# Optimization experiments

Hardware: AMD Instinct MI355X
Metric: run time of the kernel (lower is better)

Reference implementation:

```python
import jax, jax.numpy as jnp
from jax import lax
import numpy as np

EPS = 1e-8

def squash(x, axis=-1):
    sq = jnp.sum(x * x, axis=axis, keepdims=True)
    return sq / (1.0 + sq) * x / (jnp.sqrt(sq) + EPS)

def conv1d(x, w, b):
    # x: [B, Cin, L], w: [Cout, Cin, K]
    y = lax.conv_general_dilated(x, w, (1,), 'VALID',
                                 dimension_numbers=('NCH', 'OIH', 'NCH'))
    return y + b[None, :, None]

def setup_inputs() -> dict:
    key = jax.random.key(0)
    ks = jax.random.split(key, 6)
    B = 4096
    x = jax.random.normal(ks[0], (B, 50, 128), dtype=jnp.float32)
    conv1_w = jax.random.normal(ks[1], (50, 128, 9), dtype=jnp.float32) * (1.0 / np.sqrt(128 * 9))
    conv1_b = jnp.zeros((50,), dtype=jnp.float32)
    pconv_w = jax.random.normal(ks[2], (64, 42, 3), dtype=jnp.float32) * (1.0 / np.sqrt(42 * 3))
    pconv_b = jnp.zeros((64,), dtype=jnp.float32)
    W = 0.01 * jax.random.normal(ks[3], (5, 384, 16, 8), dtype=jnp.float32)
    return {"x": x, "conv1_w": conv1_w, "conv1_b": conv1_b,
            "pconv_w": pconv_w, "pconv_b": pconv_b, "W": W}

def reference(x, conv1_w, conv1_b, pconv_w, pconv_b, W):
    B = x.shape[0]
    NUM_ROUTING = 3
    # conv + relu: [B,50,128] -> [B,128,50] -> conv -> [B,50,42] -> permute -> [B,42,50]
    h = conv1d(jnp.transpose(x, (0, 2, 1)), conv1_w, conv1_b)
    h = jnp.transpose(jax.nn.relu(h), (0, 2, 1))  # [B,42,50]
    # primary caps: conv1d -> [B,64,48] -> reshape [B,384,8] -> squash
    p = conv1d(h, pconv_w, pconv_b)
    u = squash(p.reshape(B, -1, 8), axis=-1)  # [B,384,8]
    # u_hat[b,o,c,d] = W[o,c,d,i] * u[b,c,i]
    u_hat = jnp.einsum('ocdi,bci->bocd', W, u)  # [B,5,384,16]
    tu = lax.stop_gradient(u_hat)
    b = jnp.zeros((B, 5, 384, 1), dtype=u_hat.dtype)
    for _ in range(NUM_ROUTING - 1):
        c = jax.nn.softmax(b, axis=1)            # [B,5,384,1]
        s = jnp.sum(c * tu, axis=2)              # [B,5,16]
        v = squash(s)                            # [B,5,16]
        uv = jnp.einsum('bocd,bod->boc', tu, v)[..., None]
        b = b + uv
    c = jax.nn.softmax(b, axis=1)
    s = jnp.sum(c * u_hat, axis=2)
    v = squash(s)  # [B,5,16]
    return v
```

## Files before the change

### kernel.cpp

```cpp
#include <hip/hip_runtime.h>
#include <hip/hip_bf16.h>

typedef unsigned short ushort_t;
typedef _Float16 h2 __attribute__((ext_vector_type(2)));
typedef _Float16 half4_t __attribute__((ext_vector_type(4)));
typedef _Float16 half8_t __attribute__((ext_vector_type(8)));
typedef float f32x4 __attribute__((ext_vector_type(4)));
#define EPSQ 1e-8f

__device__ __forceinline__ float fdot2f(h2 a, h2 b, float c) {
#if __has_builtin(__builtin_amdgcn_fdot2)
  return __builtin_amdgcn_fdot2(a, b, c, false);
#else
  return fmaf((float)a.x, (float)b.x, fmaf((float)a.y, (float)b.y, c));
#endif
}
__device__ __forceinline__ h2 bc_h2(unsigned int v) { return __builtin_bit_cast(h2, v); }
__device__ __forceinline__ unsigned int bc_u32(h2 v) { return __builtin_bit_cast(unsigned int, v); }
__device__ __forceinline__ ushort_t bc_u16(_Float16 v) { return __builtin_bit_cast(ushort_t, v); }


__global__ __launch_bounds__(256) void k0_prep(
    const float* __restrict__ w1, const float* __restrict__ pw,
    const float* __restrict__ Wf,
    _Float16* __restrict__ wc16, _Float16* __restrict__ pwB16,
    _Float16* __restrict__ Whs)
{
  int i = blockIdx.x * 256 + threadIdx.x;
  if (i < 73728) {
    int c  = i / 8192;
    int r  = i % 8192;
    int co = r >> 7;
    int k  = r & 127;
    wc16[i] = (co < 50) ? (_Float16)w1[co*1152 + k*9 + c] : (_Float16)0.f;
  }
  if (i < 10240) {
    int co2 = i / 160, kk = i % 160;
    int k = kk / 48, ci = kk % 48;
    float v = (k < 3 && ci < 42) ? pw[co2*126 + ci*3 + k] : 0.f;
    pwB16[i] = (_Float16)v;
  }
  {
    int i8 = i & 7;
    int r  = i >> 3;
    int d  = r & 15;
    int rc = r >> 4;
    int c  = rc % 384;
    int o  = rc / 384;
    Whs[(((o*16 + d)*384) + c)*8 + i8] = (_Float16)Wf[i];
  }
}

__global__ __launch_bounds__(256) void k12_mfma(
    const float* __restrict__ x, const float* __restrict__ b1,
    const float* __restrict__ b2, const _Float16* __restrict__ wc16,
    const _Float16* __restrict__ pwB16, ushort_t* __restrict__ u16)
{
  __shared__ float smem[19728];
  _Float16* xh   = (_Float16*)smem;
  _Float16* hr16 = (_Float16*)smem;
  _Float16* pB   = (_Float16*)smem + 8736;
  float*    pbuf = smem + 9744;

  const int tid   = threadIdx.x;
  const int w     = tid >> 6;
  const int lane  = tid & 63;
  const int lc    = lane & 15;
  const int qd    = lane >> 4;
  const int gbase = blockIdx.x * 3;

  for (int j = tid; j < 4800; j += 256) {
    int g = j / 1600, r = j - g*1600;
    int p = r >> 5, q = r & 31;
    int bb = gbase + g; if (bb > 4095) bb = 4095;
    float4 v = *(const float4*)(x + bb*6400 + p*128 + q*4);
    half4_t hv = {(_Float16)v.x, (_Float16)v.y, (_Float16)v.z, (_Float16)v.w};
    *(half4_t*)(xh + g*6800 + p*136 + q*4) = hv;
  }
  {
    const uint4* wg = (const uint4*)wc16;
    uint4* dst = (uint4*)(xh + 20400);
#pragma unroll
    for (int it = 0; it < 4; ++it) {
      int f = it*256 + tid;
      dst[(f >> 4)*17 + (f & 15)] = wg[f];
    }
  }

  const _Float16* abase[2];
#pragma unroll
  for (int tm = 0; tm < 2; ++tm) {
    int m = 32*w + 16*tm + lc;
    if (m > 125) m = 125;
    int g = m / 42, l = m - g*42;
    abase[tm] = xh + g*6800 + l*136 + qd*8;
  }

  f32x4 acc[2][4];
#pragma unroll
  for (int tm = 0; tm < 2; ++tm)
#pragma unroll
    for (int tn = 0; tn < 4; ++tn)
      acc[tm][tn] = (f32x4){0.f, 0.f, 0.f, 0.f};

  __syncthreads();

  uint4 pf[4];
  for (int c = 0; c < 9; ++c) {
    if (c < 8) {
      const uint4* wg = (const uint4*)wc16 + (c + 1)*1024;
#pragma unroll
      for (int it = 0; it < 4; ++it) pf[it] = wg[it*256 + tid];
    }
    const _Float16* Bb = xh + 20400 + (c & 1)*8704;
    const _Float16* a0 = abase[0] + c*136;
    const _Float16* a1 = abase[1] + c*136;
#pragma unroll
    for (int kk = 0; kk < 128; kk += 32) {
      half8_t av0 = *(const half8_t*)(a0 + kk);
      half8_t av1 = *(const half8_t*)(a1 + kk);
#pragma unroll
      for (int tn = 0; tn < 4; ++tn) {
        half8_t bv = *(const half8_t*)(Bb + (16*tn + lc)*136 + qd*8 + kk);
        acc[0][tn] = __builtin_amdgcn_mfma_f32_16x16x32_f16(av0, bv, acc[0][tn], 0, 0, 0);
        acc[1][tn] = __builtin_amdgcn_mfma_f32_16x16x32_f16(av1, bv, acc[1][tn], 0, 0, 0);
      }
    }
    __syncthreads();
    if (c < 8) {
      uint4* dst = (uint4*)(xh + 20400 + ((c + 1) & 1)*8704);
#pragma unroll
      for (int it = 0; it < 4; ++it) {
        int f = it*256 + tid;
        dst[(f >> 4)*17 + (f & 15)] = pf[it];
      }
      __syncthreads();
    }
  }

  for (int j = tid; j < 4368; j += 256) smem[j] = 0.f;
  {
    const uint4* pg = (const uint4*)pwB16;
    uint4* dst = (uint4*)pB;
    for (int f = tid; f < 1280; f += 256) {
      int row = f / 20, cc = f - row*20;
      dst[row*21 + cc] = pg[f];
    }
  }
  __syncthreads();

#pragma unroll
  for (int tm = 0; tm < 2; ++tm) {
    int mb = 32*w + 16*tm + 4*qd;
#pragma unroll
    for (int tn = 0; tn < 4; ++tn) {
      int co = 16*tn + lc;
      if (co < 50) {
        float bias = b1[co];
#pragma unroll
        for (int r = 0; r < 4; ++r) {
          int m = mb + r;
          if (m < 126) {
            int g = m / 42, l = m - g*42;
            hr16[g*2912 + co*56 + l] = (_Float16)fmaxf(acc[tm][tn][r] + bias, 0.f);
          }
        }
      }
    }
  }
  __syncthreads();

  f32x4 acc2[3][4];
#pragma unroll
  for (int tm = 0; tm < 3; ++tm)
#pragma unroll
    for (int tn = 0; tn < 4; ++tn)
      acc2[tm][tn] = (f32x4){0.f, 0.f, 0.f, 0.f};

#pragma unroll
  for (int kc = 0; kc < 5; ++kc) {
    int kk0 = kc*32 + qd*8;
    int k   = (kk0 >= 144) ? 3 : (kk0 >= 96) ? 2 : (kk0 >= 48) ? 1 : 0;
    int ci0 = kk0 - k*48;
    half8_t bv[4];
#pragma unroll
    for (int tn = 0; tn < 4; ++tn)
      bv[tn] = *(const half8_t*)(pB + (16*tn + lc)*168 + kk0);
#pragma unroll
    for (int tm = 0; tm < 3; ++tm) {
      int T = w + 4*tm; int Tc = (T < 9) ? T : 8;
      int g = Tc/3, l2 = (Tc - g*3)*16 + lc;
      half8_t av = *(const half8_t*)(hr16 + g*2912 + (l2 + k)*56 + ci0);
#pragma unroll
      for (int tn = 0; tn < 4; ++tn)
        acc2[tm][tn] = __builtin_amdgcn_mfma_f32_16x16x32_f16(av, bv[tn], acc2[tm][tn], 0, 0, 0);
    }
  }

#pragma unroll
  for (int tm = 0; tm < 3; ++tm) {
    int T = w + 4*tm;
    if (T < 9) {
      int g = T/3, l2b = (T - g*3)*16;
#pragma unroll
      for (int tn = 0; tn < 4; ++tn) {
        int co2 = 16*tn + lc;
        float bias2 = b2[co2];
#pragma unroll
        for (int r = 0; r < 4; ++r) {
          int l2 = l2b + 4*qd + r;
          pbuf[g*3328 + co2*52 + l2] = acc2[tm][tn][r] + bias2;
        }
      }
    }
  }
  __syncthreads();

  for (int idx = tid; idx < 1152; idx += 256) {
    int g = idx / 384, cap = idx - g*384;
    int bb = gbase + g;
    if (bb < 4096) {
      int co2 = cap / 6, gg = cap - co2*6;
      const float* pp = pbuf + g*3328 + co2*52 + gg*8;
      float4 a0 = *(const float4*)pp;
      float4 a1 = *(const float4*)(pp + 4);
      float sq = a0.x*a0.x + a0.y*a0.y + a0.z*a0.z + a0.w*a0.w
               + a1.x*a1.x + a1.y*a1.y + a1.z*a1.z + a1.w*a1.w;
      float sc = sq / ((1.f + sq) * (sqrtf(sq) + EPSQ));
      h2 p0 = {(_Float16)(a0.x*sc), (_Float16)(a0.y*sc)};
      h2 p1 = {(_Float16)(a0.z*sc), (_Float16)(a0.w*sc)};
      h2 p2 = {(_Float16)(a1.x*sc), (_Float16)(a1.y*sc)};
      h2 p3 = {(_Float16)(a1.z*sc), (_Float16)(a1.w*sc)};
      *(uint4*)(u16 + ((size_t)bb*384 + cap)*8) =
          make_uint4(bc_u32(p0), bc_u32(p1), bc_u32(p2), bc_u32(p3));
    }
  }
}

__global__ __launch_bounds__(384) void k3_route(
    const ushort_t* __restrict__ u16, const _Float16* __restrict__ Whs,
    float* __restrict__ out)
{
  __shared__ __align__(16) ushort_t uhb[384][82];
  __shared__ __align__(16) float part[2][6][80];
  __shared__ __align__(16) ushort_t svh16[2][80];

  const int t    = threadIdx.x;
  const int b0   = blockIdx.x * 2;
  const int w    = t >> 6;
  const int lane = t & 63;
  const int jmap3 = ((lane & 1) << 2) | (lane & 2) | ((lane & 4) >> 2);

  h2 ua[2][4];
#pragma unroll
  for (int bb = 0; bb < 2; ++bb) {
    uint4 uu = *(const uint4*)(u16 + ((size_t)(b0 + bb)*384 + t)*8);
    ua[bb][0] = bc_h2(uu.x); ua[bb][1] = bc_h2(uu.y);
    ua[bb][2] = bc_h2(uu.z); ua[bb][3] = bc_h2(uu.w);
  }

  h2 uhreg[40];
  const uint4* wb = (const uint4*)Whs;
#pragma unroll
  for (int o = 0; o < 5; ++o) {
    const uint4* wp = wb + (size_t)(o*16)*384 + t;
#pragma unroll
    for (int dd = 0; dd < 8; ++dd) {
      uint4 w0 = wp[(size_t)(2*dd)*384];
      uint4 w1 = wp[(size_t)(2*dd + 1)*384];
      float s00 = fdot2f(bc_h2(w0.x), ua[0][0], fdot2f(bc_h2(w0.y), ua[0][1],
                  fdot2f(bc_h2(w0.z), ua[0][2], fdot2f(bc_h2(w0.w), ua[0][3], 0.f))));
      float s10 = fdot2f(bc_h2(w1.x), ua[0][0], fdot2f(bc_h2(w1.y), ua[0][1],
                  fdot2f(bc_h2(w1.z), ua[0][2], fdot2f(bc_h2(w1.w), ua[0][3], 0.f))));
      uhreg[o*8 + dd] = (h2){(_Float16)s00, (_Float16)s10};
      float s01 = fdot2f(bc_h2(w0.x), ua[1][0], fdot2f(bc_h2(w0.y), ua[1][1],
                  fdot2f(bc_h2(w0.z), ua[1][2], fdot2f(bc_h2(w0.w), ua[1][3], 0.f))));
      float s11 = fdot2f(bc_h2(w1.x), ua[1][0], fdot2f(bc_h2(w1.y), ua[1][1],
                  fdot2f(bc_h2(w1.z), ua[1][2], fdot2f(bc_h2(w1.w), ua[1][3], 0.f))));
      *(h2*)&uhb[t][o*16 + 2*dd] = (h2){(_Float16)s01, (_Float16)s11};
    }
  }

  float lg[2][5] = {{0,0,0,0,0},{0,0,0,0,0}};

  const bool s0 = (lane & 1) != 0;
  const bool s1 = (lane & 2) != 0;
  const bool s2 = (lane & 4) != 0;

  for (int it = 0; it < 3; ++it) {
    float cof[2][5];
#pragma unroll
    for (int bb = 0; bb < 2; ++bb) {
      float m = fmaxf(fmaxf(fmaxf(lg[bb][0],lg[bb][1]),fmaxf(lg[bb][2],lg[bb][3])),lg[bb][4]);
      float Z = 0.f;
#pragma unroll
      for (int o = 0; o < 5; ++o) { cof[bb][o] = __expf(lg[bb][o]-m); Z += cof[bb][o]; }
      float inv = 1.f / Z;
#pragma unroll
      for (int o = 0; o < 5; ++o) cof[bb][o] *= inv;
    }

#pragma unroll
    for (int bb = 0; bb < 2; ++bb) {
#pragma unroll
      for (int o = 0; o < 5; ++o) {
#pragma unroll
        for (int g = 0; g < 2; ++g) {
          float p[8];
#pragma unroll
          for (int m2 = 0; m2 < 4; ++m2) {
            h2 uh = (bb == 0) ? uhreg[o*8 + g*4 + m2]
                              : *(const h2*)&uhb[t][o*16 + g*8 + 2*m2];
            p[2*m2]     = cof[bb][o] * (float)uh.x;
            p[2*m2 + 1] = cof[bb][o] * (float)uh.y;
          }
          float v4[4];
#pragma unroll
          for (int i = 0; i < 4; ++i) {
            float keep = s0 ? p[i+4] : p[i];
            float send = s0 ? p[i]   : p[i+4];
            v4[i] = keep + __shfl_xor(send, 1);
          }
          float v2[2];
#pragma unroll
          for (int i = 0; i < 2; ++i) {
            float keep = s1 ? v4[i+2] : v4[i];
            float send = s1 ? v4[i]   : v4[i+2];
            v2[i] = keep + __shfl_xor(send, 2);
          }
          float v1;
          {
            float keep = s2 ? v2[1] : v2[0];
            float send = s2 ? v2[0] : v2[1];
            v1 = keep + __shfl_xor(send, 4);
          }
          v1 += __shfl_xor(v1, 8);
          v1 += __shfl_xor(v1, 16);
          v1 += __shfl_xor(v1, 32);
          if (lane < 8) part[bb][w][o*16 + g*8 + jmap3] = v1;
        }
      }
    }
    __syncthreads();

    if (t < 160) {
      int bb  = (t >= 80) ? 1 : 0;
      int idx = t - bb*80;
      float s = part[bb][0][idx] + part[bb][1][idx] + part[bb][2][idx]
              + part[bb][3][idx] + part[bb][4][idx] + part[bb][5][idx];
      float sq = s * s;
      sq += __shfl_xor(sq, 1);
      sq += __shfl_xor(sq, 2);
      sq += __shfl_xor(sq, 4);
      sq += __shfl_xor(sq, 8);
      float f = sq / ((1.f + sq) * (sqrtf(sq) + EPSQ));
      if (it == 2) out[(size_t)(b0 + bb)*80 + idx] = s * f;
      else         svh16[bb][idx] = bc_u16((_Float16)(s * f));
    }
    __syncthreads();

    if (it < 2) {
#pragma unroll
      for (int bb = 0; bb < 2; ++bb) {
#pragma unroll
        for (int o = 0; o < 5; ++o) {
          uint4 sa = *(const uint4*)&svh16[bb][o*16];
          uint4 sb = *(const uint4*)&svh16[bb][o*16 + 8];
          h2 svp[8] = {bc_h2(sa.x), bc_h2(sa.y), bc_h2(sa.z), bc_h2(sa.w),
                       bc_h2(sb.x), bc_h2(sb.y), bc_h2(sb.z), bc_h2(sb.w)};
          float dv = 0.f;
#pragma unroll
          for (int k = 0; k < 8; ++k) {
            h2 uh = (bb == 0) ? uhreg[o*8 + k]
                              : *(const h2*)&uhb[t][o*16 + 2*k];
            dv = fdot2f(uh, svp[k], dv);
          }
          lg[bb][o] += dv;
        }
      }
    }
  }
}

extern "C" void kernel_launch(void* const* d_in, const int* in_sizes, int n_in,
                              void* d_out, int out_size, void* d_ws, size_t ws_size,
                              hipStream_t stream) {
  const float* x  = (const float*)d_in[0];
  const float* w1 = (const float*)d_in[1];
  const float* b1 = (const float*)d_in[2];
  const float* pw = (const float*)d_in[3];
  const float* b2 = (const float*)d_in[4];
  const float* Wf = (const float*)d_in[5];
  float* out = (float*)d_out;
  char* ws = (char*)d_ws;

  _Float16* wc16  = (_Float16*)(ws);
  _Float16* pwB16 = (_Float16*)(ws + 147456);
  _Float16* Whs   = (_Float16*)(ws + 167936);
  ushort_t* u16   = (ushort_t*)(ws + 659456);

  k0_prep<<<960, 256, 0, stream>>>(w1, pw, Wf, wc16, pwB16, Whs);
  k12_mfma<<<1366, 256, 0, stream>>>(x, b1, b2, wc16, pwB16, u16);
  k3_route<<<2048, 384, 0, stream>>>(u16, Whs, out);
}
```

Baseline: 466.9 us.

## Route one batch per 256-thread block with uneven capsule split

The routing kernel now handles one batch element per block with 256 threads instead of two elements per 384-thread block. Threads 0-127 own two input capsules (one held in registers, one in LDS) and threads 128-255 own one. This cuts the shared-memory footprint and doubles the block count, aiming for higher occupancy. In exchange, the W fp16 weights are reloaded per batch element rather than shared across two, and the heavy threads create load imbalance between the two halves of the block.

Measured after the change: 702.9 us. +50.6%, slower.

```diff
diff --git a/kernel.cpp b/kernel.cpp
--- a/kernel.cpp
+++ b/kernel.cpp
@@ -237,71 +237,126 @@
   }
 }
 
-__global__ __launch_bounds__(384) void k3_route(
+__global__ __launch_bounds__(256) void k3_route(
     const ushort_t* __restrict__ u16, const _Float16* __restrict__ Whs,
     float* __restrict__ out)
 {
-  __shared__ __align__(16) ushort_t uhb[384][82];
-  __shared__ __align__(16) float part[2][6][80];
-  __shared__ __align__(16) ushort_t svh16[2][80];
+  __shared__ __align__(16) ushort_t uhb[128][82];
+  __shared__ __align__(16) float part[6][80];
+  __shared__ __align__(16) ushort_t svh16[80];
 
   const int t    = threadIdx.x;
-  const int b0   = blockIdx.x * 2;
+  const int b    = blockIdx.x;
   const int w    = t >> 6;
   const int lane = t & 63;
+  const bool heavy = (t < 128);
   const int jmap3 = ((lane & 1) << 2) | (lane & 2) | ((lane & 4) >> 2);
 
-  h2 ua[2][4];
-#pragma unroll
-  for (int bb = 0; bb < 2; ++bb) {
-    uint4 uu = *(const uint4*)(u16 + ((size_t)(b0 + bb)*384 + t)*8);
-    ua[bb][0] = bc_h2(uu.x); ua[bb][1] = bc_h2(uu.y);
-    ua[bb][2] = bc_h2(uu.z); ua[bb][3] = bc_h2(uu.w);
+  h2 ua0[4], ua1[4];
+  {
+    uint4 uu = *(const uint4*)(u16 + ((size_t)b*384 + t)*8);
+    ua0[0] = bc_h2(uu.x); ua0[1] = bc_h2(uu.y);
+    ua0[2] = bc_h2(uu.z); ua0[3] = bc_h2(uu.w);
+  }
+  if (heavy) {
+    uint4 uu = *(const uint4*)(u16 + ((size_t)b*384 + 256 + t)*8);
+    ua1[0] = bc_h2(uu.x); ua1[1] = bc_h2(uu.y);
+    ua1[2] = bc_h2(uu.z); ua1[3] = bc_h2(uu.w);
   }
 
   h2 uhreg[40];
   const uint4* wb = (const uint4*)Whs;
 #pragma unroll
   for (int o = 0; o < 5; ++o) {
-    const uint4* wp = wb + (size_t)(o*16)*384 + t;
 #pragma unroll
     for (int dd = 0; dd < 8; ++dd) {
-      uint4 w0 = wp[(size_t)(2*dd)*384];
-      uint4 w1 = wp[(size_t)(2*dd + 1)*384];
-      float s00 = fdot2f(bc_h2(w0.x), ua[0][0], fdot2f(bc_h2(w0.y), ua[0][1],
-                  fdot2f(bc_h2(w0.z), ua[0][2], fdot2f(bc_h2(w0.w), ua[0][3], 0.f))));
-      float s10 = fdot2f(bc_h2(w1.x), ua[0][0], fdot2f(bc_h2(w1.y), ua[0][1],
-                  fdot2f(bc_h2(w1.z), ua[0][2], fdot2f(bc_h2(w1.w), ua[0][3], 0.f))));
+      const uint4* r0 = wb + (size_t)(o*16 + 2*dd)*384;
+      const uint4* r1 = wb + (size_t)(o*16 + 2*dd + 1)*384;
+      uint4 w0 = r0[t];
+      uint4 w1 = r1[t];
+      float s00 = fdot2f(bc_h2(w0.x), ua0[0], fdot2f(bc_h2(w0.y), ua0[1],
+                  fdot2f(bc_h2(w0.z), ua0[2], fdot2f(bc_h2(w0.w), ua0[3], 0.f))));
+      float s10 = fdot2f(bc_h2(w1.x), ua0[0], fdot2f(bc_h2(w1.y), ua0[1],
+                  fdot2f(bc_h2(w1.z), ua0[2], fdot2f(bc_h2(w1.w), ua0[3], 0.f))));
       uhreg[o*8 + dd] = (h2){(_Float16)s00, (_Float16)s10};
-      float s01 = fdot2f(bc_h2(w0.x), ua[1][0], fdot2f(bc_h2(w0.y), ua[1][1],
-                  fdot2f(bc_h2(w0.z), ua[1][2], fdot2f(bc_h2(w0.w), ua[1][3], 0.f))));
-      float s11 = fdot2f(bc_h2(w1.x), ua[1][0], fdot2f(bc_h2(w1.y), ua[1][1],
-                  fdot2f(bc_h2(w1.z), ua[1][2], fdot2f(bc_h2(w1.w), ua[1][3], 0.f))));
-      *(h2*)&uhb[t][o*16 + 2*dd] = (h2){(_Float16)s01, (_Float16)s11};
-    }
-  }
-
-  float lg[2][5] = {{0,0,0,0,0},{0,0,0,0,0}};
+      if (heavy) {
+        uint4 w0b = r0[256 + t];
+        uint4 w1b = r1[256 + t];
+        float s01 = fdot2f(bc_h2(w0b.x), ua1[0], fdot2f(bc_h2(w0b.y), ua1[1],
+                    fdot2f(bc_h2(w0b.z), ua1[2], fdot2f(bc_h2(w0b.w), ua1[3], 0.f))));
+        float s11 = fdot2f(bc_h2(w1b.x), ua1[0], fdot2f(bc_h2(w1b.y), ua1[1],
+                    fdot2f(bc_h2(w1b.z), ua1[2], fdot2f(bc_h2(w1b.w), ua1[3], 0.f))));
+        *(h2*)&uhb[t][o*16 + 2*dd] = (h2){(_Float16)s01, (_Float16)s11};
+      }
+    }
+  }
+
+  float lg0[5] = {0,0,0,0,0};
+  float lg1[5] = {0,0,0,0,0};
 
   const bool s0 = (lane & 1) != 0;
   const bool s1 = (lane & 2) != 0;
   const bool s2 = (lane & 4) != 0;
 
   for (int it = 0; it < 3; ++it) {
-    float cof[2][5];
-#pragma unroll
-    for (int bb = 0; bb < 2; ++bb) {
-      float m = fmaxf(fmaxf(fmaxf(lg[bb][0],lg[bb][1]),fmaxf(lg[bb][2],lg[bb][3])),lg[bb][4]);
+    float cof0[5], cof1[5];
+    {
+      float m = fmaxf(fmaxf(fmaxf(lg0[0],lg0[1]),fmaxf(lg0[2],lg0[3])),lg0[4]);
       float Z = 0.f;
 #pragma unroll
-      for (int o = 0; o < 5; ++o) { cof[bb][o] = __expf(lg[bb][o]-m); Z += cof[bb][o]; }
+      for (int o = 0; o < 5; ++o) { cof0[o] = __expf(lg0[o]-m); Z += cof0[o]; }
       float inv = 1.f / Z;
 #pragma unroll
-      for (int o = 0; o < 5; ++o) cof[bb][o] *= inv;
-    }
-
-#pragma unroll
-    for (int bb = 0; bb < 2; ++bb) {
+      for (int o = 0; o < 5; ++o) cof0[o] *= inv;
+    }
+    if (heavy) {
+      float m = fmaxf(fmaxf(fmaxf(lg1[0],lg1[1]),fmaxf(lg1[2],lg1[3])),lg1[4]);
+      float Z = 0.f;
+#pragma unroll
+      for (int o = 0; o < 5; ++o) { cof1[o] = __expf(lg1[o]-m); Z += cof1[o]; }
+      float inv = 1.f / Z;
+#pragma unroll
+      for (int o = 0; o < 5; ++o) cof1[o] *= inv;
+    }
+
+#pragma unroll
+    for (int o = 0; o < 5; ++o) {
+#pragma unroll
+      for (int g = 0; g < 2; ++g) {
+        float p[8];
+#pragma unroll
+        for (int m2 = 0; m2 < 4; ++m2) {
+          h2 uh = uhreg[o*8 + g*4 + m2];
+          p[2*m2]     = cof0[o] * (float)uh.x;
+          p[2*m2 + 1] = cof0[o] * (float)uh.y;
+        }
+        float v4[4];
+#pragma unroll
+        for (int i = 0; i < 4; ++i) {
+          float keep = s0 ? p[i+4] : p[i];
+          float send = s0 ? p[i]   : p[i+4];
+          v4[i] = keep + __shfl_xor(send, 1);
+        }
+        float v2[2];
+#pragma unroll
+        for (int i = 0; i < 2; ++i) {
+          float keep = s1 ? v4[i+2] : v4[i];
+          float send = s1 ? v4[i]   : v4[i+2];
+          v2[i] = keep + __shfl_xor(send, 2);
+        }
+        float v1;
+        {
+          float keep = s2 ? v2[1] : v2[0];
+          float send = s2 ? v2[0] : v2[1];
+          v1 = keep + __shfl_xor(send, 4);
+        }
+        v1 += __shfl_xor(v1, 8);
+        v1 += __shfl_xor(v1, 16);
+        v1 += __shfl_xor(v1, 32);
+        if (lane < 8) part[w][o*16 + g*8 + jmap3] = v1;
+      }
+    }
+    if (heavy) {
 #pragma unroll
       for (int o = 0; o < 5; ++o) {
 #pragma unroll
@@ -309,10 +364,9 @@
           float p[8];
 #pragma unroll
           for (int m2 = 0; m2 < 4; ++m2) {
-            h2 uh = (bb == 0) ? uhreg[o*8 + g*4 + m2]
-                              : *(const h2*)&uhb[t][o*16 + g*8 + 2*m2];
-            p[2*m2]     = cof[bb][o] * (float)uh.x;
-            p[2*m2 + 1] = cof[bb][o] * (float)uh.y;
+            h2 uh = *(const h2*)&uhb[t][o*16 + g*8 + 2*m2];
+            p[2*m2]     = cof1[o] * (float)uh.x;
+            p[2*m2 + 1] = cof1[o] * (float)uh.y;
           }
           float v4[4];
 #pragma unroll
@@ -337,45 +391,43 @@
           v1 += __shfl_xor(v1, 8);
           v1 += __shfl_xor(v1, 16);
           v1 += __shfl_xor(v1, 32);
-          if (lane < 8) part[bb][w][o*16 + g*8 + jmap3] = v1;
+          if (lane < 8) part[4 + w][o*16 + g*8 + jmap3] = v1;
         }
       }
     }
     __syncthreads();
 
-    if (t < 160) {
-      int bb  = (t >= 80) ? 1 : 0;
-      int idx = t - bb*80;
-      float s = part[bb][0][idx] + part[bb][1][idx] + part[bb][2][idx]
-              + part[bb][3][idx] + part[bb][4][idx] + part[bb][5][idx];
+    if (t < 80) {
+      float s = part[0][t] + part[1][t] + part[2][t]
+              + part[3][t] + part[4][t] + part[5][t];
       float sq = s * s;
       sq += __shfl_xor(sq, 1);
       sq += __shfl_xor(sq, 2);
       sq += __shfl_xor(sq, 4);
       sq += __shfl_xor(sq, 8);
       float f = sq / ((1.f + sq) * (sqrtf(sq) + EPSQ));
-      if (it == 2) out[(size_t)(b0 + bb)*80 + idx] = s * f;
-      else         svh16[bb][idx] = bc_u16((_Float16)(s * f));
+      if (it == 2) out[(size_t)b*80 + t] = s * f;
+      else         svh16[t] = bc_u16((_Float16)(s * f));
     }
     __syncthreads();
 
     if (it < 2) {
 #pragma unroll
-      for (int bb = 0; bb < 2; ++bb) {
-#pragma unroll
-        for (int o = 0; o < 5; ++o) {
-          uint4 sa = *(const uint4*)&svh16[bb][o*16];
-          uint4 sb = *(const uint4*)&svh16[bb][o*16 + 8];
-          h2 svp[8] = {bc_h2(sa.x), bc_h2(sa.y), bc_h2(sa.z), bc_h2(sa.w),
-                       bc_h2(sb.x), bc_h2(sb.y), bc_h2(sb.z), bc_h2(sb.w)};
-          float dv = 0.f;
-#pragma unroll
-          for (int k = 0; k < 8; ++k) {
-            h2 uh = (bb == 0) ? uhreg[o*8 + k]
-                              : *(const h2*)&uhb[t][o*16 + 2*k];
-            dv = fdot2f(uh, svp[k], dv);
-          }
-          lg[bb][o] += dv;
+      for (int o = 0; o < 5; ++o) {
+        uint4 sa = *(const uint4*)&svh16[o*16];
+        uint4 sb = *(const uint4*)&svh16[o*16 + 8];
+        h2 svp[8] = {bc_h2(sa.x), bc_h2(sa.y), bc_h2(sa.z), bc_h2(sa.w),
+                     bc_h2(sb.x), bc_h2(sb.y), bc_h2(sb.z), bc_h2(sb.w)};
+        float dv = 0.f;
+#pragma unroll
+        for (int k = 0; k < 8; ++k) dv = fdot2f(uhreg[o*8 + k], svp[k], dv);
+        lg0[o] += dv;
+        if (heavy) {
+          float dv1 = 0.f;
+#pragma unroll
+          for (int k = 0; k < 8; ++k)
+            dv1 = fdot2f(*(const h2*)&uhb[t][o*16 + 2*k], svp[k], dv1);
+          lg1[o] += dv1;
         }
       }
     }
@@ -401,5 +453,5 @@
 
   k0_prep<<<960, 256, 0, stream>>>(w1, pw, Wf, wc16, pwB16, Whs);
   k12_mfma<<<1366, 256, 0, stream>>>(x, b1, b2, wc16, pwB16, u16);
-  k3_route<<<2048, 384, 0, stream>>>(u16, Whs, out);
+  k3_route<<<4096, 256, 0, stream>>>(u16, Whs, out);
 }
```
